# Kernel tuning notes

Measured on AMD Instinct MI355X. Metric: run time of the kernel, lower is better.

Reference implementation:

```python
import jax, jax.numpy as jnp
import numpy as np

N = 50000      # nodes
E = 800000     # edges (before self-loops)
G = 64         # graphs in batch
F_IN = 128
HID = 32
HEADS = 4
OUT = 10
NEG_SLOPE = 0.2  # PyG GATConv default


def setup_inputs() -> dict:
    key = jax.random.key(0)
    ks = jax.random.split(key, 16)
    x = jax.random.normal(ks[0], (N, F_IN), jnp.float32)
    edge_src = jax.random.randint(ks[1], (E,), 0, N)
    edge_dst = jax.random.randint(ks[2], (E,), 0, N)
    batch = jnp.sort(jax.random.randint(ks[3], (N,), 0, G))
    # layer 1: in -> hidden, heads=4, concat
    W1 = jax.random.normal(ks[4], (F_IN, HEADS * HID), jnp.float32) / np.sqrt(F_IN)
    att_src1 = jax.random.normal(ks[5], (HEADS, HID), jnp.float32) / np.sqrt(HID)
    att_dst1 = jax.random.normal(ks[6], (HEADS, HID), jnp.float32) / np.sqrt(HID)
    b1 = jnp.zeros((HEADS * HID,), jnp.float32)
    # layer 2: hidden*heads -> hidden, heads=1
    W2 = jax.random.normal(ks[7], (HEADS * HID, HID), jnp.float32) / np.sqrt(HEADS * HID)
    att_src2 = jax.random.normal(ks[8], (1, HID), jnp.float32) / np.sqrt(HID)
    att_dst2 = jax.random.normal(ks[9], (1, HID), jnp.float32) / np.sqrt(HID)
    b2 = jnp.zeros((HID,), jnp.float32)
    fc_w = jax.random.normal(ks[10], (HID, OUT), jnp.float32) / np.sqrt(HID)
    fc_b = jnp.zeros((OUT,), jnp.float32)
    return dict(x=x, edge_src=edge_src, edge_dst=edge_dst, batch=batch,
                W1=W1, att_src1=att_src1, att_dst1=att_dst1, b1=b1,
                W2=W2, att_src2=att_src2, att_dst2=att_dst2, b2=b2,
                fc_w=fc_w, fc_b=fc_b)


def gat_conv(x, si, di, W, a_src, a_dst, b):
    n = x.shape[0]
    H, C = a_src.shape
    h = (x @ W).reshape(n, H, C)                    # [N,H,C]
    alpha_src = jnp.sum(h * a_src, axis=-1)         # [N,H]
    alpha_dst = jnp.sum(h * a_dst, axis=-1)         # [N,H]
    logits = jax.nn.leaky_relu(alpha_src[si] + alpha_dst[di], NEG_SLOPE)  # [Et,H]
    # segment softmax grouped by destination node (self-loops => no empty segments)
    m = jax.ops.segment_max(logits, di, num_segments=n)
    e = jnp.exp(logits - m[di])
    denom = jax.ops.segment_sum(e, di, num_segments=n)
    alpha = e / denom[di]                           # [Et,H]
    out = jax.ops.segment_sum(alpha[:, :, None] * h[si], di, num_segments=n)
    return out.reshape(n, H * C) + b


def reference(x, edge_src, edge_dst, batch,
              W1, att_src1, att_dst1, b1,
              W2, att_src2, att_dst2, b2,
              fc_w, fc_b):
    n = x.shape[0]
    loops = jnp.arange(n)
    si = jnp.concatenate([edge_src, loops])   # PyG add_self_loops=True
    di = jnp.concatenate([edge_dst, loops])
    h = gat_conv(x, si, di, W1, att_src1, att_dst1, b1)
    h = jax.nn.relu(h)                         # dropout identity (eval)
    h = gat_conv(h, si, di, W2, att_src2, att_dst2, b2)
    h = jax.nn.relu(h)
    # global mean pool over graphs
    sums = jax.ops.segment_sum(h, batch, num_segments=G)
    cnt = jax.ops.segment_sum(jnp.ones((n,), h.dtype), batch, num_segments=G)
    pooled = sums / jnp.maximum(cnt, 1.0)[:, None]
    return pooled @ fc_w + fc_b
```

## Files before the change

### kernel.cpp

```cpp
#include <hip/hip_runtime.h>
#include <hip/hip_fp16.h>

#define NEG_SLOPE 0.2f
#define GN 64
#define OUTC 10
#define EPB 4096
#define NPB 512
#define REC_CAP 9984

typedef _Float16 f16x8 __attribute__((ext_vector_type(8)));
typedef float f32x4 __attribute__((ext_vector_type(4)));

__device__ __forceinline__ float lrelu(float x) { return x > 0.f ? x : NEG_SLOPE * x; }

__global__ __launch_bounds__(256) void k_gemm1(
    const float* __restrict__ x, const __half* __restrict__ W1T,
    const float* __restrict__ asrc, const float* __restrict__ adst,
    __half* __restrict__ h1, float* __restrict__ as1, float* __restrict__ ad1, int N)
{
    int wave = threadIdx.x >> 6, lane = threadIdx.x & 63;
    int row0 = blockIdx.x * 64 + wave * 16;
    int ar = row0 + (lane & 15);
    int arc = min(ar, N - 1);
    int k0 = (lane >> 4) * 8;
    const float* xr = x + (size_t)arc * 128 + k0;
    f16x8 afrag[4];
    #pragma unroll
    for (int kk = 0; kk < 4; ++kk) {
        float4 u0 = *(const float4*)(xr + kk * 32);
        float4 u1 = *(const float4*)(xr + kk * 32 + 4);
        f16x8 a;
        a[0] = (_Float16)u0.x; a[1] = (_Float16)u0.y;
        a[2] = (_Float16)u0.z; a[3] = (_Float16)u0.w;
        a[4] = (_Float16)u1.x; a[5] = (_Float16)u1.y;
        a[6] = (_Float16)u1.z; a[7] = (_Float16)u1.w;
        afrag[kk] = a;
    }
    int cl = lane & 15;
    int rbase = row0 + 4 * (lane >> 4);
    const _Float16* WT = (const _Float16*)W1T;
    float ps[4][4] = {};
    float pd[4][4] = {};
    #pragma unroll
    for (int t = 0; t < 8; ++t) {
        int col = t * 16 + cl;
        float av = asrc[col];
        float dv = adst[col];
        const _Float16* wrow = WT + (size_t)col * 128 + k0;
        f32x4 acc = {0.f, 0.f, 0.f, 0.f};
        #pragma unroll
        for (int kk = 0; kk < 4; ++kk) {
            f16x8 b = *(const f16x8*)(wrow + kk * 32);
            acc = __builtin_amdgcn_mfma_f32_16x16x32_f16(afrag[kk], b, acc, 0, 0, 0);
        }
        int h = t >> 1;
        #pragma unroll
        for (int r = 0; r < 4; ++r) {
            ps[r][h] += acc[r] * av;
            pd[r][h] += acc[r] * dv;
            int row = rbase + r;
            if (row < N)
                h1[(size_t)row * 128 + col] = __float2half_rn(acc[r]);
        }
    }
    #pragma unroll
    for (int r = 0; r < 4; ++r)
        #pragma unroll
        for (int h = 0; h < 4; ++h) {
            float a = ps[r][h], b = pd[r][h];
            #pragma unroll
            for (int m = 1; m < 16; m <<= 1) {
                a += __shfl_xor(a, m);
                b += __shfl_xor(b, m);
            }
            ps[r][h] = a; pd[r][h] = b;
        }
    if (cl == 0) {
        #pragma unroll
        for (int r = 0; r < 4; ++r) {
            int row = rbase + r;
            if (row < N) {
                ((float4*)as1)[row] = make_float4(ps[r][0], ps[r][1], ps[r][2], ps[r][3]);
                ((float4*)ad1)[row] = make_float4(pd[r][0], pd[r][1], pd[r][2], pd[r][3]);
            }
        }
    }
}

__global__ __launch_bounds__(256) void k_parta_prep(
    const int* __restrict__ di, int* __restrict__ blkcnt, int E, int nb, int nblk,
    const float* __restrict__ W1, const float* __restrict__ W2,
    __half* __restrict__ W1T, __half* __restrict__ W2T)
{
    int t = threadIdx.x;
    if (blockIdx.x >= nblk) {
        int t0 = (blockIdx.x - nblk) * 256 + t;
        for (int i = t0; i < 128 * 128; i += 16 * 256) {
            int k = i >> 7, n = i & 127;
            W1T[n * 128 + k] = __float2half_rn(W1[i]);
        }
        for (int i = t0; i < 128 * 32; i += 16 * 256) {
            int k = i >> 5, n = i & 31;
            W2T[n * 128 + k] = __float2half_rn(W2[i]);
        }
        return;
    }
    __shared__ int lcnt[128];
    for (int i = t; i < nb; i += 256) lcnt[i] = 0;
    __syncthreads();
    int base = blockIdx.x * EPB;
    #pragma unroll
    for (int k = 0; k < 16; ++k) {
        int e = base + t + k * 256;
        if (e < E) atomicAdd(&lcnt[di[e] >> 9], 1);
    }
    __syncthreads();
    for (int i = t; i < nb; i += 256) blkcnt[blockIdx.x * nb + i] = lcnt[i];
}

__global__ __launch_bounds__(256) void k_colscan(
    const int* __restrict__ blkcnt, int* __restrict__ blkbase,
    int* __restrict__ bsum, int nblk, int nb)
{
    __shared__ int s[256];
    int b = blockIdx.x, t = threadIdx.x;
    int v = (t < nblk) ? blkcnt[t * nb + b] : 0;
    s[t] = v;
    __syncthreads();
    for (int off = 1; off < 256; off <<= 1) {
        int u = (t >= off) ? s[t - off] : 0;
        __syncthreads();
        s[t] += u;
        __syncthreads();
    }
    if (t < nblk) blkbase[t * nb + b] = s[t] - v;
    if (t == 255) bsum[b] = s[255];
}

__global__ __launch_bounds__(256) void k_parta2(
    const int* __restrict__ si, const int* __restrict__ di,
    const int* __restrict__ blkbase, const int* __restrict__ bsum,
    unsigned* __restrict__ rec, int E, int nb)
{
    __shared__ int lbase[128];
    __shared__ int lcnt[128];
    __shared__ int ls[128];
    int t = threadIdx.x;
    int v = 0;
    if (t < 128) {
        v = (t < nb) ? bsum[t] : 0;
        ls[t] = v;
    }
    __syncthreads();
    for (int off = 1; off < 128; off <<= 1) {
        int u = (t < 128 && t >= off) ? ls[t - off] : 0;
        __syncthreads();
        if (t < 128) ls[t] += u;
        __syncthreads();
    }
    if (t < 128) {
        lbase[t] = (ls[t] - v) + ((t < nb) ? blkbase[blockIdx.x * nb + t] : 0);
        lcnt[t] = 0;
    }
    __syncthreads();
    int base = blockIdx.x * EPB;
    #pragma unroll
    for (int k = 0; k < 16; ++k) {
        int e = base + t + k * 256;
        if (e < E) {
            int d = di[e];
            int b = d >> 9;
            int r = atomicAdd(&lcnt[b], 1);
            rec[lbase[b] + r] = ((unsigned)(d & 511) << 17) | (unsigned)si[e];
        }
    }
}

__global__ __launch_bounds__(512) void k_partb(
    const unsigned* __restrict__ rec, const int* __restrict__ bsum,
    int* __restrict__ csr_src, int* __restrict__ row_start,
    int* __restrict__ deg, int N, int nb)
{
    __shared__ int lhist[512], lexcl[512], lcur[512];
    __shared__ unsigned lsrc[REC_CAP];
    __shared__ int gbs;
    int b = blockIdx.x, t = threadIdx.x;
    int n0 = b << 9;
    int nn = min(512, N - n0);
    if (t == 0) {
        int s = 0;
        for (int i = 0; i < b; ++i) s += bsum[i];
        gbs = s;
    }
    lhist[t] = 0;
    __syncthreads();
    int gb = gbs;
    int S = bsum[b];
    if (S > REC_CAP) S = REC_CAP;
    for (int i = t; i < S; i += 512)
        atomicAdd(&lhist[rec[gb + i] >> 17], 1);
    __syncthreads();
    int v = lhist[t];
    lexcl[t] = v;
    __syncthreads();
    for (int off = 1; off < 512; off <<= 1) {
        int u = (t >= off) ? lexcl[t - off] : 0;
        __syncthreads();
        lexcl[t] += u;
        __syncthreads();
    }
    int excl = lexcl[t] - v;
    __syncthreads();
    lexcl[t] = excl;
    lcur[t] = excl;
    __syncthreads();
    for (int i = t; i < S; i += 512) {
        unsigned r = rec[gb + i];
        int p = atomicAdd(&lcur[r >> 17], 1);
        if (p < REC_CAP) lsrc[p] = r & 0x1FFFFu;
    }
    __syncthreads();
    for (int i = t; i < S; i += 512) csr_src[gb + i] = (int)lsrc[i];
    if (t < nn) {
        deg[n0 + t] = lhist[t];
        row_start[n0 + t] = gb + lexcl[t];
    }
}

__global__ __launch_bounds__(256) void k_agg1(
    const int* __restrict__ csr_src, const int* __restrict__ row_start,
    const int* __restrict__ deg,
    const __half* __restrict__ h1, const float* __restrict__ as1,
    const float* __restrict__ ad1, __half* __restrict__ out1, int N)
{
    int idx = blockIdx.x * 256 + threadIdx.x;
    int node = idx >> 4, lane = idx & 15;
    if (node >= N) return;
    int head = lane >> 2;
    const float4* h16 = (const float4*)h1;
    float ad = ad1[4 * node + head];
    float m0 = lrelu(as1[4 * node + head] + ad);
    float den = 1.f;
    float acc[8];
    {
        float4 raw = h16[(size_t)node * 16 + lane];
        const __half2* hh = (const __half2*)&raw;
        #pragma unroll
        for (int q = 0; q < 4; ++q) {
            float2 f = __half22float2(hh[q]);
            acc[2 * q] = f.x; acc[2 * q + 1] = f.y;
        }
    }

    int e0 = row_start[node];
    int d  = deg[node];
    int nbatch = (d + 7) >> 3;

    auto LOAD = [&](int t, int s[8], float4 r[8], float& w0, float& w1) {
        int base = e0 + t * 8;
        int last = e0 + d;
        #pragma unroll
        for (int j = 0; j < 8; ++j) {
            int ix = base + j;
            s[j] = csr_src[ix < last ? ix : e0];
        }
        #pragma unroll
        for (int j = 0; j < 8; ++j) r[j] = h16[(size_t)s[j] * 16 + lane];
        int j0 = (lane & 3) * 2;
        float a0 = as1[4 * s[j0] + head];
        float a1 = as1[4 * s[j0 + 1] + head];
        w0 = __expf(lrelu(a0 + ad) - m0);
        w1 = __expf(lrelu(a1 + ad) - m0);
    };
    auto CONSUME = [&](int t, const int s[8], const float4 r[8], float w0, float w1) {
        int rem = d - t * 8;
        #pragma unroll
        for (int j = 0; j < 8; ++j) {
            int srcl = (lane & 12) | (j >> 1);
            float w = __shfl((j & 1) ? w1 : w0, srcl, 16);
            w = (j < rem) ? w : 0.f;
            den += w;
            const __half2* hh = (const __half2*)&r[j];
            #pragma unroll
            for (int q = 0; q < 4; ++q) {
                float2 g = __half22float2(hh[q]);
                acc[2 * q]     += w * g.x;
                acc[2 * q + 1] += w * g.y;
            }
        }
    };

    if (nbatch > 0) {
        int sA[8]; float4 rA[8]; float wA0, wA1;
        LOAD(0, sA, rA, wA0, wA1);
        for (int t = 0; t < nbatch - 1; ++t) {
            int sB[8]; float4 rB[8]; float wB0, wB1;
            LOAD(t + 1, sB, rB, wB0, wB1);
            CONSUME(t, sA, rA, wA0, wA1);
            #pragma unroll
            for (int j = 0; j < 8; ++j) { sA[j] = sB[j]; rA[j] = rB[j]; }
            wA0 = wB0; wA1 = wB1;
        }
        CONSUME(nbatch - 1, sA, rA, wA0, wA1);
    }

    float inv = 1.f / den;
    __half2 o[4];
    #pragma unroll
    for (int q = 0; q < 4; ++q)
        o[q] = __floats2half2_rn(acc[2 * q] * inv, acc[2 * q + 1] * inv);
    ((float4*)out1)[(size_t)node * 16 + lane] = *(float4*)o;
}

__global__ __launch_bounds__(256) void k_gemm2(
    const __half* __restrict__ out1h, const float* __restrict__ b1,
    const __half* __restrict__ W2T, const float* __restrict__ asrc2,
    const float* __restrict__ adst2, __half* __restrict__ h2,
    float* __restrict__ as2, float* __restrict__ ad2, int N)
{
    int wave = threadIdx.x >> 6, lane = threadIdx.x & 63;
    int row0 = blockIdx.x * 64 + wave * 16;
    int ar = row0 + (lane & 15);
    int arc = min(ar, N - 1);
    int k0 = (lane >> 4) * 8;
    const __half* xr = out1h + (size_t)arc * 128 + k0;
    const float* br = b1 + k0;
    f16x8 afrag[4];
    #pragma unroll
    for (int kk = 0; kk < 4; ++kk) {
        float4 raw = *(const float4*)(xr + kk * 32);
        const __half2* hh = (const __half2*)&raw;
        float4 c0 = *(const float4*)(br + kk * 32);
        float4 c1 = *(const float4*)(br + kk * 32 + 4);
        float bb[8] = {c0.x, c0.y, c0.z, c0.w, c1.x, c1.y, c1.z, c1.w};
        f16x8 a;
        #pragma unroll
        for (int j = 0; j < 4; ++j) {
            float2 f = __half22float2(hh[j]);
            a[2 * j]     = (_Float16)fmaxf(f.x + bb[2 * j], 0.f);
            a[2 * j + 1] = (_Float16)fmaxf(f.y + bb[2 * j + 1], 0.f);
        }
        afrag[kk] = a;
    }
    int cl = lane & 15;
    int rbase = row0 + 4 * (lane >> 4);
    const _Float16* WT = (const _Float16*)W2T;
    float ps[4] = {}, pd[4] = {};
    #pragma unroll
    for (int t = 0; t < 2; ++t) {
        int col = t * 16 + cl;
        float av = asrc2[col];
        float dv = adst2[col];
        const _Float16* wrow = WT + (size_t)col * 128 + k0;
        f32x4 acc = {0.f, 0.f, 0.f, 0.f};
        #pragma unroll
        for (int kk = 0; kk < 4; ++kk) {
            f16x8 b = *(const f16x8*)(wrow + kk * 32);
            acc = __builtin_amdgcn_mfma_f32_16x16x32_f16(afrag[kk], b, acc, 0, 0, 0);
        }
        #pragma unroll
        for (int r = 0; r < 4; ++r) {
            ps[r] += acc[r] * av;
            pd[r] += acc[r] * dv;
            int row = rbase + r;
            if (row < N)
                h2[(size_t)row * 32 + col] = __float2half_rn(acc[r]);
        }
    }
    #pragma unroll
    for (int r = 0; r < 4; ++r) {
        float a = ps[r], b = pd[r];
        #pragma unroll
        for (int m = 1; m < 16; m <<= 1) {
            a += __shfl_xor(a, m);
            b += __shfl_xor(b, m);
        }
        if (cl == 0) {
            int row = rbase + r;
            if (row < N) { as2[row] = a; ad2[row] = b; }
        }
    }
}

__global__ __launch_bounds__(256) void k_agg2(
    const int* __restrict__ csr_src, const int* __restrict__ row_start,
    const int* __restrict__ deg,
    const __half* __restrict__ h2, const float* __restrict__ as2,
    const float* __restrict__ ad2, __half* __restrict__ out2, int N)
{
    int idx = blockIdx.x * 256 + threadIdx.x;
    int node = idx >> 3, lane = idx & 7;
    if (node >= N) return;
    const float2* hv = (const float2*)h2;
    float ad = ad2[node];
    float m0 = lrelu(as2[node] + ad);
    float den = 1.f;
    float acc[4];
    {
        float2 raw = hv[(size_t)node * 8 + lane];
        const __half2* hh = (const __half2*)&raw;
        float2 f0 = __half22float2(hh[0]);
        float2 f1 = __half22float2(hh[1]);
        acc[0] = f0.x; acc[1] = f0.y; acc[2] = f1.x; acc[3] = f1.y;
    }

    int e0 = row_start[node];
    int d  = deg[node];
    int nbatch = (d + 7) >> 3;

    auto LOAD = [&](int t, int s[8], float2 r[8], float& wv) {
        int base = e0 + t * 8;
        int last = e0 + d;
        #pragma unroll
        for (int j = 0; j < 8; ++j) {
            int ix = base + j;
            s[j] = csr_src[ix < last ? ix : e0];
        }
        #pragma unroll
        for (int j = 0; j < 8; ++j) r[j] = hv[(size_t)s[j] * 8 + lane];
        float a = as2[s[lane]];
        wv = __expf(lrelu(a + ad) - m0);
    };
    auto CONSUME = [&](int t, const int s[8], const float2 r[8], float wv) {
        int rem = d - t * 8;
        #pragma unroll
        for (int j = 0; j < 8; ++j) {
            float w = __shfl(wv, j, 8);
            w = (j < rem) ? w : 0.f;
            den += w;
            const __half2* hh = (const __half2*)&r[j];
            float2 g0 = __half22float2(hh[0]);
            float2 g1 = __half22float2(hh[1]);
            acc[0] += w * g0.x; acc[1] += w * g0.y;
            acc[2] += w * g1.x; acc[3] += w * g1.y;
        }
    };

    if (nbatch > 0) {
        int sA[8]; float2 rA[8]; float wA;
        LOAD(0, sA, rA, wA);
        for (int t = 0; t < nbatch - 1; ++t) {
            int sB[8]; float2 rB[8]; float wB;
            LOAD(t + 1, sB, rB, wB);
            CONSUME(t, sA, rA, wA);
            #pragma unroll
            for (int j = 0; j < 8; ++j) { sA[j] = sB[j]; rA[j] = rB[j]; }
            wA = wB;
        }
        CONSUME(nbatch - 1, sA, rA, wA);
    }

    float inv = 1.f / den;
    __half2 o0 = __floats2half2_rn(acc[0] * inv, acc[1] * inv);
    __half2 o1 = __floats2half2_rn(acc[2] * inv, acc[3] * inv);
    float2 pk;
    *(__half2*)&pk.x = o0;
    *(__half2*)&pk.y = o1;
    ((float2*)out2)[(size_t)node * 8 + lane] = pk;
}

__global__ __launch_bounds__(256) void k_pool(
    const __half* __restrict__ out2, const float* __restrict__ b2,
    const int* __restrict__ batch, float* __restrict__ partial, int N)
{
    int g = blockIdx.x >> 2, chunkid = blockIdx.x & 3;
    int lo = 0, hi = N;
    while (lo < hi) { int mid = (lo + hi) >> 1; if (batch[mid] < g) lo = mid + 1; else hi = mid; }
    int start = lo;
    hi = N;
    while (lo < hi) { int mid = (lo + hi) >> 1; if (batch[mid] < g + 1) lo = mid + 1; else hi = mid; }
    int end = lo;
    int len = end - start;
    int chunk = (len + 3) >> 2;
    int s0 = start + chunkid * chunk;
    int s1 = min(s0 + chunk, end);

    int tid = threadIdx.x;
    int c = tid & 31, r = tid >> 5;
    float bias = b2[c];
    float acc = 0.f;
    for (int i = s0 + r; i < s1; i += 8)
        acc += fmaxf(__half2float(out2[(size_t)i * 32 + c]) + bias, 0.f);
    __shared__ float s[8][32];
    s[r][c] = acc;
    __syncthreads();
    if (r == 0) {
        float v = s[0][c] + s[1][c] + s[2][c] + s[3][c] +
                  s[4][c] + s[5][c] + s[6][c] + s[7][c];
        partial[(size_t)blockIdx.x * 32 + c] = v;
    }
}

__global__ __launch_bounds__(256) void k_fc(
    const float* __restrict__ partial, const int* __restrict__ batch,
    const float* __restrict__ fc_w, const float* __restrict__ fc_b,
    float* __restrict__ out, int N)
{
    __shared__ float pooled[GN][32];
    __shared__ float cnts[GN];
    int t = threadIdx.x;
    for (int idx = t; idx < GN * 32; idx += 256) {
        int g = idx >> 5, c = idx & 31;
        pooled[g][c] = partial[(g * 4 + 0) * 32 + c] + partial[(g * 4 + 1) * 32 + c] +
                       partial[(g * 4 + 2) * 32 + c] + partial[(g * 4 + 3) * 32 + c];
    }
    if (t < GN) {
        int g = t;
        int lo = 0, hi = N;
        while (lo < hi) { int mid = (lo + hi) >> 1; if (batch[mid] < g) lo = mid + 1; else hi = mid; }
        int start = lo;
        hi = N;
        while (lo < hi) { int mid = (lo + hi) >> 1; if (batch[mid] < g + 1) lo = mid + 1; else hi = mid; }
        cnts[g] = fmaxf((float)(lo - start), 1.f);
    }
    __syncthreads();
    for (int idx = t; idx < GN * OUTC; idx += 256) {
        int g = idx / OUTC, o = idx % OUTC;
        float inv = 1.f / cnts[g];
        float a = fc_b[o];
        #pragma unroll
        for (int c = 0; c < 32; ++c)
            a += pooled[g][c] * inv * fc_w[c * OUTC + o];
        out[idx] = a;
    }
}

extern "C" void kernel_launch(void* const* d_in, const int* in_sizes, int n_in,
                              void* d_out, int out_size, void* d_ws, size_t ws_size,
                              hipStream_t stream)
{
    const float* x        = (const float*)d_in[0];
    const int*   esrc     = (const int*)d_in[1];
    const int*   edst     = (const int*)d_in[2];
    const int*   batch    = (const int*)d_in[3];
    const float* W1       = (const float*)d_in[4];
    const float* att_src1 = (const float*)d_in[5];
    const float* att_dst1 = (const float*)d_in[6];
    const float* b1       = (const float*)d_in[7];
    const float* W2       = (const float*)d_in[8];
    const float* att_src2 = (const float*)d_in[9];
    const float* att_dst2 = (const float*)d_in[10];
    const float* b2       = (const float*)d_in[11];
    const float* fc_w     = (const float*)d_in[12];
    const float* fc_b     = (const float*)d_in[13];
    int N = in_sizes[3];
    int E = in_sizes[1];
    float* out = (float*)d_out;

    int nb   = (N + NPB - 1) >> 9;
    int nblk = (E + EPB - 1) / EPB;

    float*    base  = (float*)d_ws;
    __half*   h1    = (__half*)base;
    float*    as1   = base + (size_t)N * 64;
    float*    ad1   = as1 + (size_t)N * 4;
    __half*   out1  = (__half*)(ad1 + (size_t)N * 4);
    __half*   h2    = (__half*)(ad1 + (size_t)N * 4 + (size_t)N * 64);
    float*    as2   = ad1 + (size_t)N * 4 + (size_t)N * 64 + (size_t)N * 16;
    float*    ad2   = as2 + N;
    __half*   out2  = (__half*)(ad2 + N);
    float*    partial = ad2 + N + (size_t)N * 16;
    int*      deg       = (int*)(partial + GN * 4 * 32);
    int*      row_start = deg + N;
    int*      csr_src   = row_start + N;
    unsigned* rec       = (unsigned*)(csr_src + E);
    int*      blkcnt    = (int*)(rec + E);
    int*      blkbase   = blkcnt + (size_t)nblk * nb;
    int*      bsum      = blkbase + (size_t)nblk * nb;
    __half*   W1T       = (__half*)(bsum + nb);
    __half*   W2T       = W1T + 128 * 128;

    int nb_row = (N + 63) / 64;

    k_parta_prep<<<nblk + 16, 256, 0, stream>>>(edst, blkcnt, E, nb, nblk, W1, W2, W1T, W2T);
    k_colscan<<<nb,   256, 0, stream>>>(blkcnt, blkbase, bsum, nblk, nb);
    k_parta2 <<<nblk, 256, 0, stream>>>(esrc, edst, blkbase, bsum, rec, E, nb);
    k_partb  <<<nb,   512, 0, stream>>>(rec, bsum, csr_src, row_start, deg, N, nb);

    k_gemm1<<<nb_row, 256, 0, stream>>>(x, W1T, att_src1, att_dst1, h1, as1, ad1, N);
    k_agg1 <<<(N * 16 + 255) / 256, 256, 0, stream>>>(csr_src, row_start, deg, h1, as1, ad1, out1, N);

    k_gemm2<<<nb_row, 256, 0, stream>>>(out1, b1, W2T, att_src2, att_dst2, h2, as2, ad2, N);
    k_agg2 <<<(N * 8 + 255) / 256, 256, 0, stream>>>(csr_src, row_start, deg, h2, as2, ad2, out2, N);

    k_pool<<<GN * 4, 256, 0, stream>>>(out2, b2, batch, partial, N);
    k_fc  <<<1, 256, 0, stream>>>(partial, batch, fc_w, fc_b, out, N);
}
```

Measured before the change: 149.1 us.

## Fuse gemm1 into edge-partition kernel and precompute per-bucket record bases

Measured after the change: 136.6 us. -8.4%, faster.

```diff
diff --git a/kernel.cpp b/kernel.cpp
--- a/kernel.cpp
+++ b/kernel.cpp
@@ -13,80 +13,6 @@
 
 __device__ __forceinline__ float lrelu(float x) { return x > 0.f ? x : NEG_SLOPE * x; }
 
-__global__ __launch_bounds__(256) void k_gemm1(
-    const float* __restrict__ x, const __half* __restrict__ W1T,
-    const float* __restrict__ asrc, const float* __restrict__ adst,
-    __half* __restrict__ h1, float* __restrict__ as1, float* __restrict__ ad1, int N)
-{
-    int wave = threadIdx.x >> 6, lane = threadIdx.x & 63;
-    int row0 = blockIdx.x * 64 + wave * 16;
-    int ar = row0 + (lane & 15);
-    int arc = min(ar, N - 1);
-    int k0 = (lane >> 4) * 8;
-    const float* xr = x + (size_t)arc * 128 + k0;
-    f16x8 afrag[4];
-    #pragma unroll
-    for (int kk = 0; kk < 4; ++kk) {
-        float4 u0 = *(const float4*)(xr + kk * 32);
-        float4 u1 = *(const float4*)(xr + kk * 32 + 4);
-        f16x8 a;
-        a[0] = (_Float16)u0.x; a[1] = (_Float16)u0.y;
-        a[2] = (_Float16)u0.z; a[3] = (_Float16)u0.w;
-        a[4] = (_Float16)u1.x; a[5] = (_Float16)u1.y;
-        a[6] = (_Float16)u1.z; a[7] = (_Float16)u1.w;
-        afrag[kk] = a;
-    }
-    int cl = lane & 15;
-    int rbase = row0 + 4 * (lane >> 4);
-    const _Float16* WT = (const _Float16*)W1T;
-    float ps[4][4] = {};
-    float pd[4][4] = {};
-    #pragma unroll
-    for (int t = 0; t < 8; ++t) {
-        int col = t * 16 + cl;
-        float av = asrc[col];
-        float dv = adst[col];
-        const _Float16* wrow = WT + (size_t)col * 128 + k0;
-        f32x4 acc = {0.f, 0.f, 0.f, 0.f};
-        #pragma unroll
-        for (int kk = 0; kk < 4; ++kk) {
-            f16x8 b = *(const f16x8*)(wrow + kk * 32);
-            acc = __builtin_amdgcn_mfma_f32_16x16x32_f16(afrag[kk], b, acc, 0, 0, 0);
-        }
-        int h = t >> 1;
-        #pragma unroll
-        for (int r = 0; r < 4; ++r) {
-            ps[r][h] += acc[r] * av;
-            pd[r][h] += acc[r] * dv;
-            int row = rbase + r;
-            if (row < N)
-                h1[(size_t)row * 128 + col] = __float2half_rn(acc[r]);
-        }
-    }
-    #pragma unroll
-    for (int r = 0; r < 4; ++r)
-        #pragma unroll
-        for (int h = 0; h < 4; ++h) {
-            float a = ps[r][h], b = pd[r][h];
-            #pragma unroll
-            for (int m = 1; m < 16; m <<= 1) {
-                a += __shfl_xor(a, m);
-                b += __shfl_xor(b, m);
-            }
-            ps[r][h] = a; pd[r][h] = b;
-        }
-    if (cl == 0) {
-        #pragma unroll
-        for (int r = 0; r < 4; ++r) {
-            int row = rbase + r;
-            if (row < N) {
-                ((float4*)as1)[row] = make_float4(ps[r][0], ps[r][1], ps[r][2], ps[r][3]);
-                ((float4*)ad1)[row] = make_float4(pd[r][0], pd[r][1], pd[r][2], pd[r][3]);
-            }
-        }
-    }
-}
-
 __global__ __launch_bounds__(256) void k_parta_prep(
     const int* __restrict__ di, int* __restrict__ blkcnt, int E, int nb, int nblk,
     const float* __restrict__ W1, const float* __restrict__ W2,
@@ -137,14 +63,90 @@
     if (t == 255) bsum[b] = s[255];
 }
 
-__global__ __launch_bounds__(256) void k_parta2(
+__global__ __launch_bounds__(256) void k_parta2_gemm1(
     const int* __restrict__ si, const int* __restrict__ di,
     const int* __restrict__ blkbase, const int* __restrict__ bsum,
-    unsigned* __restrict__ rec, int E, int nb)
-{
-    __shared__ int lbase[128];
-    __shared__ int lcnt[128];
-    __shared__ int ls[128];
+    unsigned* __restrict__ rec, int* __restrict__ recbase, int E, int nb, int nblk,
+    const float* __restrict__ x, const __half* __restrict__ W1T,
+    const float* __restrict__ asrc, const float* __restrict__ adst,
+    __half* __restrict__ h1, float* __restrict__ as1, float* __restrict__ ad1, int N)
+{
+    __shared__ int smem[384];
+    if (blockIdx.x >= nblk) {
+        int blk = blockIdx.x - nblk;
+        int wave = threadIdx.x >> 6, lane = threadIdx.x & 63;
+        int row0 = blk * 64 + wave * 16;
+        int ar = row0 + (lane & 15);
+        int arc = min(ar, N - 1);
+        int k0 = (lane >> 4) * 8;
+        const float* xr = x + (size_t)arc * 128 + k0;
+        f16x8 afrag[4];
+        #pragma unroll
+        for (int kk = 0; kk < 4; ++kk) {
+            float4 u0 = *(const float4*)(xr + kk * 32);
+            float4 u1 = *(const float4*)(xr + kk * 32 + 4);
+            f16x8 a;
+            a[0] = (_Float16)u0.x; a[1] = (_Float16)u0.y;
+            a[2] = (_Float16)u0.z; a[3] = (_Float16)u0.w;
+            a[4] = (_Float16)u1.x; a[5] = (_Float16)u1.y;
+            a[6] = (_Float16)u1.z; a[7] = (_Float16)u1.w;
+            afrag[kk] = a;
+        }
+        int cl = lane & 15;
+        int rbase = row0 + 4 * (lane >> 4);
+        const _Float16* WT = (const _Float16*)W1T;
+        float ps[4][4] = {};
+        float pd[4][4] = {};
+        #pragma unroll
+        for (int t = 0; t < 8; ++t) {
+            int col = t * 16 + cl;
+            float av = asrc[col];
+            float dv = adst[col];
+            const _Float16* wrow = WT + (size_t)col * 128 + k0;
+            f32x4 acc = {0.f, 0.f, 0.f, 0.f};
+            #pragma unroll
+            for (int kk = 0; kk < 4; ++kk) {
+                f16x8 b = *(const f16x8*)(wrow + kk * 32);
+                acc = __builtin_amdgcn_mfma_f32_16x16x32_f16(afrag[kk], b, acc, 0, 0, 0);
+            }
+            int h = t >> 1;
+            #pragma unroll
+            for (int r = 0; r < 4; ++r) {
+                ps[r][h] += acc[r] * av;
+                pd[r][h] += acc[r] * dv;
+                int row = rbase + r;
+                if (row < N)
+                    h1[(size_t)row * 128 + col] = __float2half_rn(acc[r]);
+            }
+        }
+        #pragma unroll
+        for (int r = 0; r < 4; ++r)
+            #pragma unroll
+            for (int h = 0; h < 4; ++h) {
+                float a = ps[r][h], b = pd[r][h];
+                #pragma unroll
+                for (int m = 1; m < 16; m <<= 1) {
+                    a += __shfl_xor(a, m);
+                    b += __shfl_xor(b, m);
+                }
+                ps[r][h] = a; pd[r][h] = b;
+            }
+        if (cl == 0) {
+            #pragma unroll
+            for (int r = 0; r < 4; ++r) {
+                int row = rbase + r;
+                if (row < N) {
+                    ((float4*)as1)[row] = make_float4(ps[r][0], ps[r][1], ps[r][2], ps[r][3]);
+                    ((float4*)ad1)[row] = make_float4(pd[r][0], pd[r][1], pd[r][2], pd[r][3]);
+                }
+            }
+        }
+        return;
+    }
+
+    int* ls    = smem;
+    int* lbase = smem + 128;
+    int* lcnt  = smem + 256;
     int t = threadIdx.x;
     int v = 0;
     if (t < 128) {
@@ -162,6 +164,7 @@
         lbase[t] = (ls[t] - v) + ((t < nb) ? blkbase[blockIdx.x * nb + t] : 0);
         lcnt[t] = 0;
     }
+    if (blockIdx.x == 0 && t < nb) recbase[t] = ls[t] - v;
     __syncthreads();
     int base = blockIdx.x * EPB;
     #pragma unroll
@@ -178,25 +181,20 @@
 
 __global__ __launch_bounds__(512) void k_partb(
     const unsigned* __restrict__ rec, const int* __restrict__ bsum,
+    const int* __restrict__ recbase,
     int* __restrict__ csr_src, int* __restrict__ row_start,
     int* __restrict__ deg, int N, int nb)
 {
     __shared__ int lhist[512], lexcl[512], lcur[512];
     __shared__ unsigned lsrc[REC_CAP];
-    __shared__ int gbs;
     int b = blockIdx.x, t = threadIdx.x;
     int n0 = b << 9;
     int nn = min(512, N - n0);
-    if (t == 0) {
-        int s = 0;
-        for (int i = 0; i < b; ++i) s += bsum[i];
-        gbs = s;
-    }
-    lhist[t] = 0;
-    __syncthreads();
-    int gb = gbs;
+    int gb = recbase[b];
     int S = bsum[b];
     if (S > REC_CAP) S = REC_CAP;
+    lhist[t] = 0;
+    __syncthreads();
     for (int i = t; i < S; i += 512)
         atomicAdd(&lhist[rec[gb + i] >> 17], 1);
     __syncthreads();
@@ -567,21 +565,23 @@
     int*      blkcnt    = (int*)(rec + E);
     int*      blkbase   = blkcnt + (size_t)nblk * nb;
     int*      bsum      = blkbase + (size_t)nblk * nb;
-    __half*   W1T       = (__half*)(bsum + nb);
+    int*      recbase   = bsum + nb;
+    __half*   W1T       = (__half*)(recbase + nb);
     __half*   W2T       = W1T + 128 * 128;
 
     int nb_row = (N + 63) / 64;
 
     k_parta_prep<<<nblk + 16, 256, 0, stream>>>(edst, blkcnt, E, nb, nblk, W1, W2, W1T, W2T);
-    k_colscan<<<nb,   256, 0, stream>>>(blkcnt, blkbase, bsum, nblk, nb);
-    k_parta2 <<<nblk, 256, 0, stream>>>(esrc, edst, blkbase, bsum, rec, E, nb);
-    k_partb  <<<nb,   512, 0, stream>>>(rec, bsum, csr_src, row_start, deg, N, nb);
-
-    k_gemm1<<<nb_row, 256, 0, stream>>>(x, W1T, att_src1, att_dst1, h1, as1, ad1, N);
-    k_agg1 <<<(N * 16 + 255) / 256, 256, 0, stream>>>(csr_src, row_start, deg, h1, as1, ad1, out1, N);
+    k_colscan<<<nb, 256, 0, stream>>>(blkcnt, blkbase, bsum, nblk, nb);
+    k_parta2_gemm1<<<nblk + nb_row, 256, 0, stream>>>(
+        esrc, edst, blkbase, bsum, rec, recbase, E, nb, nblk,
+        x, W1T, att_src1, att_dst1, h1, as1, ad1, N);
+    k_partb<<<nb, 512, 0, stream>>>(rec, bsum, recbase, csr_src, row_start, deg, N, nb);
+
+    k_agg1<<<(N * 16 + 255) / 256, 256, 0, stream>>>(csr_src, row_start, deg, h1, as1, ad1, out1, N);
 
     k_gemm2<<<nb_row, 256, 0, stream>>>(out1, b1, W2T, att_src2, att_dst2, h2, as2, ad2, N);
-    k_agg2 <<<(N * 8 + 255) / 256, 256, 0, stream>>>(csr_src, row_start, deg, h2, as2, ad2, out2, N);
+    k_agg2<<<(N * 8 + 255) / 256, 256, 0, stream>>>(csr_src, row_start, deg, h2, as2, ad2, out2, N);
 
     k_pool<<<GN * 4, 256, 0, stream>>>(out2, b2, batch, partial, N);
     k_fc  <<<1, 256, 0, stream>>>(partial, batch, fc_w, fc_b, out, N);
```
